# Kernel tuning notes

Measured on AMD Instinct MI355X. Metric: run time of the kernel, lower is better.

## Reference

```python
import jax, jax.numpy as jnp
import numpy as np

N_NODES = 50000
N_EDGES = 1600000
NFEAT = 512
NHID = 64
H1 = 8      # nheads[0]
H2 = 1      # nheads[1]
NCLASS = 16
ALPHA = 0.2  # leaky_relu negative slope


def setup_inputs() -> dict:
    key = jax.random.key(0)
    ks = jax.random.split(key, 6)
    x = jax.random.normal(ks[0], (N_NODES, NFEAT), jnp.float32)
    edge_index = jax.random.randint(ks[1], (2, N_EDGES), 0, N_NODES, jnp.int32)

    def glorot(k, shape):
        fan_in, fan_out = shape[-2], shape[-1]
        std = (2.0 / (fan_in + fan_out)) ** 0.5
        return jax.random.normal(k, shape, jnp.float32) * std

    W1 = glorot(ks[2], (H1, NFEAT, NHID))
    a1 = jax.random.normal(ks[3], (H1, 2 * NHID), jnp.float32) * 0.1
    W2 = glorot(ks[4], (H2, NHID * H1, NCLASS))
    a2 = jax.random.normal(ks[5], (H2, 2 * NCLASS), jnp.float32) * 0.1
    return {"x": x, "edge_index": edge_index, "W1": W1, "a1": a1, "W2": W2, "a2": a2}


def _spgat_head(x, W, a, src, dst, n_nodes, apply_elu):
    # Sparse GAT head (pyGAT SpGraphAttentionLayer, eval mode / no dropout).
    h = x @ W                              # [N, F']
    f = W.shape[1]
    # a . [h_src || h_dst] decomposed into per-node scores (same math, no [E,2F'] concat)
    s_src = h @ a[:f]                      # [N]
    s_dst = h @ a[f:]                      # [N]
    logits = s_src[src] + s_dst[dst]       # [E]
    e = jnp.exp(-jax.nn.leaky_relu(logits, ALPHA))  # edge_e = exp(-leakyrelu(...)) > 0
    rowsum = jax.ops.segment_sum(e, src, num_segments=n_nodes)            # [N]
    agg = jax.ops.segment_sum(e[:, None] * h[dst], src, num_segments=n_nodes)  # [N, F']
    h_prime = agg / rowsum[:, None]
    return jax.nn.elu(h_prime) if apply_elu else h_prime


def reference(x, edge_index, W1, a1, W2, a2):
    src, dst = edge_index[0], edge_index[1]
    n = x.shape[0]
    # Layer 1: H1 heads, concat=True (elu inside each head), concatenated on features
    h = jnp.concatenate(
        [_spgat_head(x, W1[i], a1[i], src, dst, n, True) for i in range(W1.shape[0])],
        axis=1,
    )  # [N, H1*NHID]
    # Layer 2: H2 heads, concat=False, stacked then averaged
    outs = jnp.stack(
        [_spgat_head(h, W2[i], a2[i], src, dst, n, False) for i in range(W2.shape[0])],
        axis=2,
    )  # [N, NCLASS, H2]
    out = jnp.mean(outs, axis=2)
    return jax.nn.log_softmax(jax.nn.elu(out), axis=1)
```

## Files before the change

### kernel.cpp

```cpp
#include <hip/hip_runtime.h>

#define NN 50000
#define NE 1600000
#define NFEAT 512
#define NHID 64
#define H1 8
#define NCLASS 16
#define ALPHA 0.2f

#define BUCKETS 391
#define CAP 6144
#define EPB 4096
#define PASSA_BLKS 391
#define PASSB_BLKS 391
#define PACK_BLKS 1024
#define PACK2_BLKS 32
#define GEMM_BLKS (4 * 391)

typedef __attribute__((ext_vector_type(8))) short short8;
typedef __attribute__((ext_vector_type(4))) float floatx4;
typedef __attribute__((ext_vector_type(2))) float floatx2;

__device__ __forceinline__ float elu_f(float x) { return x > 0.0f ? x : expf(x) - 1.0f; }
__device__ __forceinline__ float edge_w(float logit) {
    return expf(-fmaxf(logit, ALPHA * logit));
}
__device__ __forceinline__ ushort f2bf(float f) {
    uint u = __float_as_uint(f);
    return (ushort)((u + 0x7FFFu + ((u >> 16) & 1)) >> 16);
}
__device__ __forceinline__ uint packbf2(float lo, float hi) {
    return (uint)f2bf(lo) | ((uint)f2bf(hi) << 16);
}
__device__ __forceinline__ float bf2f(ushort v) { return __uint_as_float((uint)v << 16); }
__device__ __forceinline__ unsigned char f2fp8(float v) {
    return (unsigned char)(__builtin_amdgcn_cvt_pk_fp8_f32(v, v, 0, false) & 0xFF);
}
__device__ __forceinline__ uint pack4fp8(float a, float b, float c, float d) {
    uint u = __builtin_amdgcn_cvt_pk_fp8_f32(a, b, 0, false);
    return __builtin_amdgcn_cvt_pk_fp8_f32(c, d, u, true);
}

__device__ __forceinline__ int scan256x(int v, int tid, int* wsum, int* tot) {
    int s = v;
#pragma unroll
    for (int o = 1; o < 64; o <<= 1) {
        int u = __shfl_up(s, o);
        if ((tid & 63) >= o) s += u;
    }
    __syncthreads();
    if ((tid & 63) == 63) wsum[tid >> 6] = s;
    __syncthreads();
    int off = 0, t = 0;
#pragma unroll
    for (int i = 0; i < 4; i++) {
        int x = wsum[i];
        if (i < (tid >> 6)) off += x;
        t += x;
    }
    *tot = t;
    return s - v + off;
}

__global__ __launch_bounds__(256) void prep_k(const float* __restrict__ W1,
                                              unsigned char* __restrict__ Wt8,
                                              const float* __restrict__ W2,
                                              ushort* __restrict__ W2tb,
                                              const int* __restrict__ ei,
                                              int* __restrict__ bucket_cnt,
                                              uint* __restrict__ staging) {
    int b = blockIdx.x;
    if (b < PACK_BLKS) {
        int i = b * 256 + threadIdx.x;
        int c = i >> 9, k = i & 511;
        Wt8[i] = f2fp8(W1[((c >> 6) * 512 + k) * 64 + (c & 63)]);
        return;
    }
    if (b < PACK_BLKS + PACK2_BLKS) {
        int i = (b - PACK_BLKS) * 256 + threadIdx.x;
        int c = i >> 9, f = i & 511;
        W2tb[i] = f2bf(W2[f * 16 + c]);
        return;
    }
    __shared__ int histA[BUCKETS];
    __shared__ int exclA[BUCKETS];
    __shared__ int baseA[BUCKETS];
    __shared__ int wsumA[4];
    __shared__ uint ebuf[EPB];
    const int blk = b - PACK_BLKS - PACK2_BLKS;
    const int t = threadIdx.x;
    const int e0 = blk * EPB;
    const int cntb = min(EPB, NE - e0);
    for (int i = t; i < BUCKETS; i += 256) histA[i] = 0;
    __syncthreads();
    int br[16]; uint pay[16];
#pragma unroll
    for (int i = 0; i < 16; i++) {
        int e = e0 + i * 256 + t;
        br[i] = -1;
        if (e < NE) {
            int s = ei[e], d = ei[NE + e];
            int bu = s >> 7;
            pay[i] = ((uint)bu << 23) | ((uint)(s & 127) << 16) | (uint)d;
            br[i] = (bu << 12) | atomicAdd(&histA[bu], 1);
        }
    }
    __syncthreads();
    int tot0, tot1;
    int v0 = histA[t];
    int v1 = (t + 256 < BUCKETS) ? histA[t + 256] : 0;
    int p0 = scan256x(v0, t, wsumA, &tot0);
    int p1 = scan256x(v1, t, wsumA, &tot1);
    exclA[t] = p0;
    if (t + 256 < BUCKETS) exclA[t + 256] = p1 + tot0;
    __syncthreads();
    for (int i = t; i < BUCKETS; i += 256) {
        int c = histA[i];
        if (c > 0) baseA[i] = atomicAdd(&bucket_cnt[i], c);
    }
#pragma unroll
    for (int i = 0; i < 16; i++)
        if (br[i] >= 0) ebuf[exclA[br[i] >> 12] + (br[i] & 4095)] = pay[i];
    __syncthreads();
    for (int j = t; j < cntb; j += 256) {
        uint v = ebuf[j];
        int bu = v >> 23;
        int pos = baseA[bu] + (j - exclA[bu]);
        staging[(size_t)bu * CAP + pos] = v;
    }
}

__global__ __launch_bounds__(64) void scan_k(const int* __restrict__ bucket_cnt,
                                             int* __restrict__ bucket_start,
                                             int* __restrict__ rowptr) {
    const int lane = threadIdx.x;
    int c[7]; int s0 = 0;
#pragma unroll
    for (int i = 0; i < 7; i++) {
        int b = lane * 7 + i;
        c[i] = (b < BUCKETS) ? bucket_cnt[b] : 0;
        s0 += c[i];
    }
    int sc = s0;
#pragma unroll
    for (int o = 1; o < 64; o <<= 1) {
        int u = __shfl_up(sc, o);
        if (lane >= o) sc += u;
    }
    int run = sc - s0;
#pragma unroll
    for (int i = 0; i < 7; i++) {
        int b = lane * 7 + i;
        if (b < BUCKETS) bucket_start[b] = run;
        run += c[i];
    }
    if (lane == 63) { bucket_start[BUCKETS] = run; rowptr[NN] = run; }
}

__global__ __launch_bounds__(256) void passb_gemm1_k(const int* __restrict__ bucket_cnt,
                                                     const int* __restrict__ bucket_start,
                                                     const uint* __restrict__ staging,
                                                     ushort* __restrict__ csru,
                                                     int* __restrict__ rowptr,
                                                     const float* __restrict__ x,
                                                     const unsigned char* __restrict__ Wt8,
                                                     const float* __restrict__ a1,
                                                     unsigned char* __restrict__ h8,
                                                     float* __restrict__ s1s,
                                                     float* __restrict__ s1d) {
    __shared__ unsigned char As[128 * 32];
    __shared__ unsigned char Bs[128 * 32];
    const int tid = threadIdx.x;

    if (blockIdx.x < PASSB_BLKS) {
        __shared__ int hist2[128], excl2[128], cur2[128], wsum2[4];
        const int b = blockIdx.x;
        const int cnt = bucket_cnt[b];
        const int sbase = bucket_start[b];
        const uint* sg = staging + (size_t)b * CAP;
        if (tid < 128) { hist2[tid] = 0; cur2[tid] = 0; }
        __syncthreads();
        for (int e = tid; e < cnt; e += 256) atomicAdd(&hist2[(sg[e] >> 16) & 127], 1);
        __syncthreads();
        int v = (tid < 128) ? hist2[tid] : 0;
        int tot;
        int ex = scan256x(v, tid, wsum2, &tot);
        if (tid < 128) {
            excl2[tid] = ex;
            int n = b * 128 + tid;
            if (n < NN) rowptr[n] = sbase + ex;
        }
        __syncthreads();
        for (int e = tid; e < cnt; e += 256) {
            uint u = sg[e];
            int sl = (u >> 16) & 127;
            int pos = excl2[sl] + atomicAdd(&cur2[sl], 1);
            csru[sbase + pos] = (ushort)(u & 0xFFFF);
        }
        return;
    }

    const int gb = blockIdx.x - PASSB_BLKS;
    const int col0 = (gb & 3) * 128;
    const int row0 = (gb >> 2) * 128;
    const int wv = tid >> 6, lane = tid & 63;
    const int quad = lane >> 4, l16 = lane & 15;
    const int sm = tid >> 2, sk = (tid & 3) * 8;
    floatx4 acc[2][8];
#pragma unroll
    for (int rt = 0; rt < 2; rt++)
#pragma unroll
        for (int ct = 0; ct < 8; ct++) acc[rt][ct] = (floatx4){0.f, 0.f, 0.f, 0.f};

    for (int k0 = 0; k0 < 512; k0 += 32) {
#pragma unroll
        for (int p = 0; p < 2; p++) {
            int r = row0 + sm + p * 64;
            float4 f0 = {}, f1 = {};
            if (r < NN) {
                const float* xp = x + (size_t)r * 512 + k0 + sk;
                f0 = *(const float4*)xp;
                f1 = *(const float4*)(xp + 4);
            }
            uint2 av;
            av.x = pack4fp8(f0.x, f0.y, f0.z, f0.w);
            av.y = pack4fp8(f1.x, f1.y, f1.z, f1.w);
            *(uint2*)(As + (sm + p * 64) * 32 + sk) = av;
            int c = col0 + sm + p * 64;
            uint2 bv = *(const uint2*)(Wt8 + (size_t)c * 512 + k0 + sk);
            *(uint2*)(Bs + (sm + p * 64) * 32 + sk) = bv;
        }
        __syncthreads();
        long a0 = *(const long*)(As + (wv * 32 + l16) * 32 + quad * 8);
        long a1f = *(const long*)(As + (wv * 32 + 16 + l16) * 32 + quad * 8);
#pragma unroll
        for (int ct = 0; ct < 8; ct++) {
            long bf = *(const long*)(Bs + (ct * 16 + l16) * 32 + quad * 8);
            acc[0][ct] = __builtin_amdgcn_mfma_f32_16x16x32_fp8_fp8(a0, bf, acc[0][ct], 0, 0, 0);
            acc[1][ct] = __builtin_amdgcn_mfma_f32_16x16x32_fp8_fp8(a1f, bf, acc[1][ct], 0, 0, 0);
        }
        __syncthreads();
    }

#pragma unroll
    for (int rt = 0; rt < 2; rt++) {
        const int rbase = row0 + wv * 32 + rt * 16 + quad * 4;
        float ss[2][4] = {}, sd[2][4] = {};
#pragma unroll
        for (int ct = 0; ct < 8; ct++) {
            int colg = col0 + ct * 16 + l16;
            int head = colg >> 6;
            int hh = ct >> 2;
            float avs = a1[head * 128 + (colg & 63)];
            float avd = a1[head * 128 + 64 + (colg & 63)];
#pragma unroll
            for (int r = 0; r < 4; r++) {
                float v = acc[rt][ct][r];
                ss[hh][r] += v * avs;
                sd[hh][r] += v * avd;
                int row = rbase + r;
                if (row < NN) h8[(size_t)row * 512 + colg] = f2fp8(v);
            }
        }
#pragma unroll
        for (int hh = 0; hh < 2; hh++)
#pragma unroll
            for (int r = 0; r < 4; r++) {
                float a_ = ss[hh][r], b_ = sd[hh][r];
#pragma unroll
                for (int o = 1; o < 16; o <<= 1) {
                    a_ += __shfl_xor(a_, o);
                    b_ += __shfl_xor(b_, o);
                }
                int row = rbase + r;
                if (l16 == 0 && row < NN) {
                    int head = (col0 >> 6) + hh;
                    s1s[row * 8 + head] = a_;
                    s1d[row * 8 + head] = b_;
                }
            }
    }
}

__global__ __launch_bounds__(256) void agg1f_k(const int* __restrict__ rowptr,
                                               const ushort* __restrict__ csru,
                                               const float* __restrict__ s1s,
                                               const float* __restrict__ s1d,
                                               const uint2* __restrict__ hb8,
                                               const ushort* __restrict__ W2tb,
                                               const float* __restrict__ a2,
                                               ushort* __restrict__ h2b,
                                               float* __restrict__ s2s,
                                               float* __restrict__ s2d) {
    __shared__ ushort Ash[16 * 512];
    const int tid = threadIdx.x;
    const int wv = tid >> 6, lane = tid & 63;
    const int n0 = blockIdx.x * 4;
    const int n = n0 + wv;
    const int head8 = lane >> 3;
    const int esub = lane & 7;
    const int beg = rowptr[n];
    const int deg = rowptr[n + 1] - beg;
    const float ssrc = s1s[n * 8 + head8];
    floatx2 acc[4] = {};
    float rsum = 0.f;

    int k = 0;
    for (; k + 8 <= deg; k += 8) {
        int dA = csru[beg + k + esub];
        float wA = edge_w(ssrc + s1d[dA * 8 + head8]);
        rsum += wA;
        int dj[8];
#pragma unroll
        for (int j = 0; j < 8; j++) dj[j] = __shfl(dA, j);
        uint2 v[8];
#pragma unroll
        for (int j = 0; j < 8; j++) v[j] = hb8[(uint)dj[j] * 64 + lane];
#pragma unroll
        for (int j = 0; j < 8; j++) {
            float wj = __shfl(wA, (head8 << 3) + j);
            floatx2 w2 = (floatx2){wj, wj};
            acc[0] += w2 * __builtin_amdgcn_cvt_pk_f32_fp8(v[j].x, false);
            acc[1] += w2 * __builtin_amdgcn_cvt_pk_f32_fp8(v[j].x, true);
            acc[2] += w2 * __builtin_amdgcn_cvt_pk_f32_fp8(v[j].y, false);
            acc[3] += w2 * __builtin_amdgcn_cvt_pk_f32_fp8(v[j].y, true);
        }
    }
    if (k < deg) {
        int jc = min(k + esub, deg - 1);
        int dwj = csru[beg + jc];
        float w = edge_w(ssrc + s1d[dwj * 8 + head8]);
        if (k + esub >= deg) w = 0.f;
        rsum += w;
        int rem = deg - k;
        for (int j = 0; j < rem; j++) {
            int djs = __shfl(dwj, j);
            uint2 vv = hb8[(uint)djs * 64 + lane];
            float wj = __shfl(w, (head8 << 3) + j);
            floatx2 w2 = (floatx2){wj, wj};
            acc[0] += w2 * __builtin_amdgcn_cvt_pk_f32_fp8(vv.x, false);
            acc[1] += w2 * __builtin_amdgcn_cvt_pk_f32_fp8(vv.x, true);
            acc[2] += w2 * __builtin_amdgcn_cvt_pk_f32_fp8(vv.y, false);
            acc[3] += w2 * __builtin_amdgcn_cvt_pk_f32_fp8(vv.y, true);
        }
    }

    rsum += __shfl_xor(rsum, 1);
    rsum += __shfl_xor(rsum, 2);
    rsum += __shfl_xor(rsum, 4);
    float inv = 1.0f / rsum;
    uint4 o;
    o.x = packbf2(elu_f(acc[0][0] * inv), elu_f(acc[0][1] * inv));
    o.y = packbf2(elu_f(acc[1][0] * inv), elu_f(acc[1][1] * inv));
    o.z = packbf2(elu_f(acc[2][0] * inv), elu_f(acc[2][1] * inv));
    o.w = packbf2(elu_f(acc[3][0] * inv), elu_f(acc[3][1] * inv));
    *(uint4*)(Ash + wv * 512 + lane * 8) = o;
    __syncthreads();

    if (wv == 0) {
        const int l16 = lane & 15, q = lane >> 4;
        floatx4 c2 = (floatx4){0.f, 0.f, 0.f, 0.f};
#pragma unroll
        for (int s = 0; s < 16; s++) {
            short8 af = *(const short8*)(Ash + l16 * 512 + s * 32 + q * 8);
            short8 bf = *(const short8*)(W2tb + l16 * 512 + s * 32 + q * 8);
            c2 = __builtin_amdgcn_mfma_f32_16x16x32_bf16(af, bf, c2, 0, 0, 0);
        }
        if (q == 0) {
#pragma unroll
            for (int r = 0; r < 4; r++) h2b[(size_t)(n0 + r) * 16 + l16] = f2bf(c2[r]);
        }
#pragma unroll
        for (int r = 0; r < 4; r++) {
            float ssv = c2[r] * a2[l16];
            float sdv = c2[r] * a2[16 + l16];
#pragma unroll
            for (int oo = 1; oo < 16; oo <<= 1) {
                ssv += __shfl_xor(ssv, oo);
                sdv += __shfl_xor(sdv, oo);
            }
            if (lane == 0) { s2s[n0 + r] = ssv; s2d[n0 + r] = sdv; }
        }
    }
}

__global__ __launch_bounds__(256) void agg2_k(const int* __restrict__ rowptr,
                                              const ushort* __restrict__ csru,
                                              const float* __restrict__ s2s,
                                              const float* __restrict__ s2d,
                                              const ushort* __restrict__ h2b,
                                              float* __restrict__ out) {
    const int n = (blockIdx.x * 256 + threadIdx.x) >> 6;
    const int lane = threadIdx.x & 63;
    if (n >= NN) return;
    const int beg = rowptr[n], end = rowptr[n + 1];
    const float sn = s2s[n];
    const int sub = lane >> 4, f = lane & 15;
    float acc = 0.f, rsum = 0.f;
    int e = beg + sub;
    for (; e + 12 < end; e += 16) {
        int d0 = csru[e], d1 = csru[e + 4], d2 = csru[e + 8], d3 = csru[e + 12];
        float t0 = s2d[d0], t1 = s2d[d1], t2 = s2d[d2], t3 = s2d[d3];
        float g0 = bf2f(h2b[(uint)d0 * 16 + f]), g1 = bf2f(h2b[(uint)d1 * 16 + f]);
        float g2 = bf2f(h2b[(uint)d2 * 16 + f]), g3 = bf2f(h2b[(uint)d3 * 16 + f]);
        float w0 = edge_w(sn + t0), w1 = edge_w(sn + t1);
        float w2 = edge_w(sn + t2), w3 = edge_w(sn + t3);
        acc += w0 * g0 + w1 * g1 + w2 * g2 + w3 * g3;
        rsum += w0 + w1 + w2 + w3;
    }
    for (; e < end; e += 4) {
        int d0 = csru[e];
        float w0 = edge_w(sn + s2d[d0]);
        acc += w0 * bf2f(h2b[(uint)d0 * 16 + f]);
        rsum += w0;
    }
    acc += __shfl_down(acc, 32);
    acc += __shfl_down(acc, 16);
    rsum += __shfl_down(rsum, 32);
    rsum += __shfl_down(rsum, 16);
    if (lane < 16) {
        float v = elu_f(acc / rsum);
        float m = v;
#pragma unroll
        for (int o = 8; o > 0; o >>= 1) m = fmaxf(m, __shfl_xor(m, o));
        float ex = expf(v - m), s = ex;
#pragma unroll
        for (int o = 8; o > 0; o >>= 1) s += __shfl_xor(s, o);
        out[(size_t)n * 16 + f] = v - (logf(s) + m);
    }
}

extern "C" void kernel_launch(void* const* d_in, const int* in_sizes, int n_in,
                              void* d_out, int out_size, void* d_ws, size_t ws_size,
                              hipStream_t stream) {
    const float* x  = (const float*)d_in[0];
    const int*   ei = (const int*)d_in[1];
    const float* W1 = (const float*)d_in[2];
    const float* a1 = (const float*)d_in[3];
    const float* W2 = (const float*)d_in[4];
    const float* a2 = (const float*)d_in[5];
    float* out = (float*)d_out;

    unsigned char* h8  = (unsigned char*)d_ws;
    unsigned char* Wt8 = h8 + (size_t)NN * 512;
    ushort* W2tb  = (ushort*)(Wt8 + 512 * 512);
    float* s1s    = (float*)(W2tb + 8192);
    float* s1d    = s1s + (size_t)NN * H1;
    int* rowptr   = (int*)(s1d + (size_t)NN * H1);
    int* bucket_cnt   = rowptr + 50056;
    int* bucket_start = bucket_cnt + 512;
    ushort* csru  = (ushort*)(bucket_start + 512);
    ushort* h2b   = csru + NE;
    float* s2s    = (float*)(h2b + (size_t)NN * 16);
    float* s2d    = s2s + NN;
    uint* staging = (uint*)(s2d + NN);

    hipMemsetAsync(bucket_cnt, 0, 512 * sizeof(int), stream);

    prep_k<<<PACK_BLKS + PACK2_BLKS + PASSA_BLKS, 256, 0, stream>>>(W1, Wt8, W2, W2tb,
                                                                    ei, bucket_cnt, staging);
    scan_k<<<1, 64, 0, stream>>>(bucket_cnt, bucket_start, rowptr);
    passb_gemm1_k<<<PASSB_BLKS + GEMM_BLKS, 256, 0, stream>>>(bucket_cnt, bucket_start,
                                                              staging, csru, rowptr,
                                                              x, Wt8, a1, h8, s1s, s1d);
    agg1f_k<<<NN / 4, 256, 0, stream>>>(rowptr, csru, s1s, s1d,
                                        (const uint2*)h8, W2tb, a2, h2b, s2s, s2d);
    agg2_k<<<(NN + 3) / 4, 256, 0, stream>>>(rowptr, csru, s2s, s2d, h2b, out);
}
```

Before: 430.7 us.

## Pre-convert x to swizzled fp8 and restructure GEMM1 with direct-to-LDS loads

Adds a prep stage that converts x to fp8 once, in an XOR-swizzled layout, into the h8 buffer. The first GEMM is restructured so each 512-thread block computes all 512 output columns for 128 rows, with K-steps of 64, using global_load_lds to stream A and B tiles straight into shared memory. It then writes h8 in place over the x8 buffer. The aim is to stop re-reading and re-converting fp32 x for each column block and to cut LDS bank conflicts, at the cost of an extra fp8 write and read pass plus 128 accumulator registers per thread, which lowers occupancy.

```diff
diff --git a/kernel.cpp b/kernel.cpp
--- a/kernel.cpp
+++ b/kernel.cpp
@@ -15,11 +15,14 @@
 #define PASSB_BLKS 391
 #define PACK_BLKS 1024
 #define PACK2_BLKS 32
-#define GEMM_BLKS (4 * 391)
+#define X8_BLKS 6250
+#define GEMMB 391
+#define NROW_PAD 50048
 
 typedef __attribute__((ext_vector_type(8))) short short8;
 typedef __attribute__((ext_vector_type(4))) float floatx4;
 typedef __attribute__((ext_vector_type(2))) float floatx2;
+typedef __attribute__((ext_vector_type(2))) long longx2;
 
 __device__ __forceinline__ float elu_f(float x) { return x > 0.0f ? x : expf(x) - 1.0f; }
 __device__ __forceinline__ float edge_w(float logit) {
@@ -40,6 +43,11 @@
     uint u = __builtin_amdgcn_cvt_pk_fp8_f32(a, b, 0, false);
     return __builtin_amdgcn_cvt_pk_fp8_f32(c, d, u, true);
 }
+
+#define GLD16(g, l)                                                              \
+    __builtin_amdgcn_global_load_lds(                                            \
+        (const __attribute__((address_space(1))) unsigned int*)(g),              \
+        (__attribute__((address_space(3))) unsigned int*)(l), 16, 0, 0)
 
 __device__ __forceinline__ int scan256x(int v, int tid, int* wsum, int* tot) {
     int s = v;
@@ -62,17 +70,43 @@
     return s - v + off;
 }
 
+__device__ __forceinline__ int scan512x(int v, int tid, int* wsum, int* tot) {
+    int s = v;
+#pragma unroll
+    for (int o = 1; o < 64; o <<= 1) {
+        int u = __shfl_up(s, o);
+        if ((tid & 63) >= o) s += u;
+    }
+    __syncthreads();
+    if ((tid & 63) == 63) wsum[tid >> 6] = s;
+    __syncthreads();
+    int off = 0, t = 0;
+#pragma unroll
+    for (int i = 0; i < 8; i++) {
+        int x = wsum[i];
+        if (i < (tid >> 6)) off += x;
+        t += x;
+    }
+    *tot = t;
+    return s - v + off;
+}
+
 __global__ __launch_bounds__(256) void prep_k(const float* __restrict__ W1,
                                               unsigned char* __restrict__ Wt8,
                                               const float* __restrict__ W2,
                                               ushort* __restrict__ W2tb,
+                                              const float* __restrict__ x,
+                                              unsigned char* x8,
                                               const int* __restrict__ ei,
                                               int* __restrict__ bucket_cnt,
                                               uint* __restrict__ staging) {
     int b = blockIdx.x;
     if (b < PACK_BLKS) {
         int i = b * 256 + threadIdx.x;
-        int c = i >> 9, k = i & 511;
+        int c = i >> 9, o = i & 511;
+        int c6 = o >> 6, qhi = (o >> 4) & 3, kb = (o >> 3) & 1, bb = o & 7;
+        int quad = qhi ^ ((c >> 1) & 3);
+        int k = c6 * 64 + kb * 32 + quad * 8 + bb;
         Wt8[i] = f2fp8(W1[((c >> 6) * 512 + k) * 64 + (c & 63)]);
         return;
     }
@@ -82,12 +116,32 @@
         W2tb[i] = f2bf(W2[f * 16 + c]);
         return;
     }
+    if (b < PACK_BLKS + PACK2_BLKS + X8_BLKS) {
+        int i = (b - PACK_BLKS - PACK2_BLKS) * 256 + threadIdx.x;
+        int row = i >> 5;
+        int o0 = (i & 31) * 16;
+        int c6 = o0 >> 6;
+        int qhi = (o0 >> 4) & 3;
+        int quad = qhi ^ ((row >> 1) & 3);
+        const float* xp = x + (size_t)row * 512 + c6 * 64 + quad * 8;
+        float4 v0 = *(const float4*)xp;
+        float4 v1 = *(const float4*)(xp + 4);
+        float4 v2 = *(const float4*)(xp + 32);
+        float4 v3 = *(const float4*)(xp + 36);
+        uint4 ov;
+        ov.x = pack4fp8(v0.x, v0.y, v0.z, v0.w);
+        ov.y = pack4fp8(v1.x, v1.y, v1.z, v1.w);
+        ov.z = pack4fp8(v2.x, v2.y, v2.z, v2.w);
+        ov.w = pack4fp8(v3.x, v3.y, v3.z, v3.w);
+        *(uint4*)(x8 + (size_t)row * 512 + o0) = ov;
+        return;
+    }
     __shared__ int histA[BUCKETS];
     __shared__ int exclA[BUCKETS];
     __shared__ int baseA[BUCKETS];
     __shared__ int wsumA[4];
     __shared__ uint ebuf[EPB];
-    const int blk = b - PACK_BLKS - PACK2_BLKS;
+    const int blk = b - PACK_BLKS - PACK2_BLKS - X8_BLKS;
     const int t = threadIdx.x;
     const int e0 = blk * EPB;
     const int cntb = min(EPB, NE - e0);
@@ -157,41 +211,42 @@
     if (lane == 63) { bucket_start[BUCKETS] = run; rowptr[NN] = run; }
 }
 
-__global__ __launch_bounds__(256) void passb_gemm1_k(const int* __restrict__ bucket_cnt,
+__global__ __launch_bounds__(512) void passb_gemm1_k(const int* __restrict__ bucket_cnt,
                                                      const int* __restrict__ bucket_start,
                                                      const uint* __restrict__ staging,
                                                      ushort* __restrict__ csru,
                                                      int* __restrict__ rowptr,
-                                                     const float* __restrict__ x,
                                                      const unsigned char* __restrict__ Wt8,
                                                      const float* __restrict__ a1,
-                                                     unsigned char* __restrict__ h8,
+                                                     unsigned char* h8x8,
                                                      float* __restrict__ s1s,
                                                      float* __restrict__ s1d) {
-    __shared__ unsigned char As[128 * 32];
-    __shared__ unsigned char Bs[128 * 32];
+    __shared__ unsigned char shmem[40960];
     const int tid = threadIdx.x;
 
     if (blockIdx.x < PASSB_BLKS) {
-        __shared__ int hist2[128], excl2[128], cur2[128], wsum2[4];
+        int* hist2 = (int*)shmem;
+        int* excl2 = hist2 + 128;
+        int* cur2 = excl2 + 128;
+        int* wsum2 = cur2 + 128;
         const int b = blockIdx.x;
         const int cnt = bucket_cnt[b];
         const int sbase = bucket_start[b];
         const uint* sg = staging + (size_t)b * CAP;
         if (tid < 128) { hist2[tid] = 0; cur2[tid] = 0; }
         __syncthreads();
-        for (int e = tid; e < cnt; e += 256) atomicAdd(&hist2[(sg[e] >> 16) & 127], 1);
+        for (int e = tid; e < cnt; e += 512) atomicAdd(&hist2[(sg[e] >> 16) & 127], 1);
         __syncthreads();
         int v = (tid < 128) ? hist2[tid] : 0;
         int tot;
-        int ex = scan256x(v, tid, wsum2, &tot);
+        int ex = scan512x(v, tid, wsum2, &tot);
         if (tid < 128) {
             excl2[tid] = ex;
             int n = b * 128 + tid;
             if (n < NN) rowptr[n] = sbase + ex;
         }
         __syncthreads();
-        for (int e = tid; e < cnt; e += 256) {
+        for (int e = tid; e < cnt; e += 512) {
             uint u = sg[e];
             int sl = (u >> 16) & 127;
             int pos = excl2[sl] + atomicAdd(&cur2[sl], 1);
@@ -200,85 +255,76 @@
         return;
     }
 
+    unsigned char* As = shmem;
+    unsigned char* Bs = shmem + 8192;
     const int gb = blockIdx.x - PASSB_BLKS;
-    const int col0 = (gb & 3) * 128;
-    const int row0 = (gb >> 2) * 128;
+    const int row0 = gb * 128;
     const int wv = tid >> 6, lane = tid & 63;
-    const int quad = lane >> 4, l16 = lane & 15;
-    const int sm = tid >> 2, sk = (tid & 3) * 8;
-    floatx4 acc[2][8];
-#pragma unroll
-    for (int rt = 0; rt < 2; rt++)
-#pragma unroll
-        for (int ct = 0; ct < 8; ct++) acc[rt][ct] = (floatx4){0.f, 0.f, 0.f, 0.f};
-
-    for (int k0 = 0; k0 < 512; k0 += 32) {
-#pragma unroll
-        for (int p = 0; p < 2; p++) {
-            int r = row0 + sm + p * 64;
-            float4 f0 = {}, f1 = {};
-            if (r < NN) {
-                const float* xp = x + (size_t)r * 512 + k0 + sk;
-                f0 = *(const float4*)xp;
-                f1 = *(const float4*)(xp + 4);
+    const int l16 = lane & 15, quad = lane >> 4;
+    const int qoff = ((quad ^ ((l16 >> 1) & 3)) << 4);
+    const int mA = wv * 16 + (lane >> 2);
+    const int offA = (lane & 3) * 16;
+    const unsigned char* gA = h8x8 + (size_t)(row0 + mA) * 512 + offA;
+    const unsigned char* gB0 = Wt8 + (size_t)(0 * 128 + mA) * 512 + offA;
+    const unsigned char* gB1 = Wt8 + (size_t)(1 * 128 + mA) * 512 + offA;
+    const unsigned char* gB2 = Wt8 + (size_t)(2 * 128 + mA) * 512 + offA;
+    const unsigned char* gB3 = Wt8 + (size_t)(3 * 128 + mA) * 512 + offA;
+
+    floatx4 acc[32];
+#pragma unroll
+    for (int ct = 0; ct < 32; ct++) acc[ct] = (floatx4){0.f, 0.f, 0.f, 0.f};
+
+    for (int k0 = 0; k0 < 512; k0 += 64) {
+        GLD16(gA + k0, As + wv * 1024);
+        GLD16(gB0 + k0, Bs + wv * 1024);
+        GLD16(gB1 + k0, Bs + 8192 + wv * 1024);
+        GLD16(gB2 + k0, Bs + 16384 + wv * 1024);
+        GLD16(gB3 + k0, Bs + 24576 + wv * 1024);
+        __syncthreads();
+        longx2 av = *(const longx2*)(As + (wv * 16 + l16) * 64 + qoff);
+        const unsigned char* bp = Bs + l16 * 64 + qoff;
+#pragma unroll
+        for (int ct = 0; ct < 32; ct++) {
+            longx2 bv = *(const longx2*)(bp + ct * 1024);
+            acc[ct] = __builtin_amdgcn_mfma_f32_16x16x32_fp8_fp8(av.x, bv.x, acc[ct], 0, 0, 0);
+            acc[ct] = __builtin_amdgcn_mfma_f32_16x16x32_fp8_fp8(av.y, bv.y, acc[ct], 0, 0, 0);
+        }
+        __syncthreads();
+    }
+
+    const int rbase = row0 + wv * 16 + quad * 4;
+#pragma unroll
+    for (int hh = 0; hh < 8; hh++) {
+        float ss[4] = {0.f, 0.f, 0.f, 0.f}, sd[4] = {0.f, 0.f, 0.f, 0.f};
+#pragma unroll
+        for (int c4 = 0; c4 < 4; c4++) {
+            int ct = hh * 4 + c4;
+            int colg = ct * 16 + l16;
+            float avs = a1[hh * 128 + c4 * 16 + l16];
+            float avd = a1[hh * 128 + 64 + c4 * 16 + l16];
+#pragma unroll
+            for (int r = 0; r < 4; r++) {
+                float v = acc[ct][r];
+                ss[r] += v * avs;
+                sd[r] += v * avd;
+                int row = rbase + r;
+                if (row < NN) h8x8[(size_t)row * 512 + colg] = f2fp8(v);
             }
-            uint2 av;
-            av.x = pack4fp8(f0.x, f0.y, f0.z, f0.w);
-            av.y = pack4fp8(f1.x, f1.y, f1.z, f1.w);
-            *(uint2*)(As + (sm + p * 64) * 32 + sk) = av;
-            int c = col0 + sm + p * 64;
-            uint2 bv = *(const uint2*)(Wt8 + (size_t)c * 512 + k0 + sk);
-            *(uint2*)(Bs + (sm + p * 64) * 32 + sk) = bv;
-        }
-        __syncthreads();
-        long a0 = *(const long*)(As + (wv * 32 + l16) * 32 + quad * 8);
-        long a1f = *(const long*)(As + (wv * 32 + 16 + l16) * 32 + quad * 8);
-#pragma unroll
-        for (int ct = 0; ct < 8; ct++) {
-            long bf = *(const long*)(Bs + (ct * 16 + l16) * 32 + quad * 8);
-            acc[0][ct] = __builtin_amdgcn_mfma_f32_16x16x32_fp8_fp8(a0, bf, acc[0][ct], 0, 0, 0);
-            acc[1][ct] = __builtin_amdgcn_mfma_f32_16x16x32_fp8_fp8(a1f, bf, acc[1][ct], 0, 0, 0);
-        }
-        __syncthreads();
-    }
-
-#pragma unroll
-    for (int rt = 0; rt < 2; rt++) {
-        const int rbase = row0 + wv * 32 + rt * 16 + quad * 4;
-        float ss[2][4] = {}, sd[2][4] = {};
-#pragma unroll
-        for (int ct = 0; ct < 8; ct++) {
-            int colg = col0 + ct * 16 + l16;
-            int head = colg >> 6;
-            int hh = ct >> 2;
-            float avs = a1[head * 128 + (colg & 63)];
-            float avd = a1[head * 128 + 64 + (colg & 63)];
-#pragma unroll
-            for (int r = 0; r < 4; r++) {
-                float v = acc[rt][ct][r];
-                ss[hh][r] += v * avs;
-                sd[hh][r] += v * avd;
-                int row = rbase + r;
-                if (row < NN) h8[(size_t)row * 512 + colg] = f2fp8(v);
+        }
+#pragma unroll
+        for (int r = 0; r < 4; r++) {
+            float a_ = ss[r], b_ = sd[r];
+#pragma unroll
+            for (int o = 1; o < 16; o <<= 1) {
+                a_ += __shfl_xor(a_, o);
+                b_ += __shfl_xor(b_, o);
             }
-        }
-#pragma unroll
-        for (int hh = 0; hh < 2; hh++)
-#pragma unroll
-            for (int r = 0; r < 4; r++) {
-                float a_ = ss[hh][r], b_ = sd[hh][r];
-#pragma unroll
-                for (int o = 1; o < 16; o <<= 1) {
-                    a_ += __shfl_xor(a_, o);
-                    b_ += __shfl_xor(b_, o);
-                }
-                int row = rbase + r;
-                if (l16 == 0 && row < NN) {
-                    int head = (col0 >> 6) + hh;
-                    s1s[row * 8 + head] = a_;
-                    s1d[row * 8 + head] = b_;
-                }
+            int row = rbase + r;
+            if (l16 == 0 && row < NN) {
+                s1s[row * 8 + hh] = a_;
+                s1d[row * 8 + hh] = b_;
             }
+        }
     }
 }
 
@@ -442,7 +488,7 @@
     float* out = (float*)d_out;
 
     unsigned char* h8  = (unsigned char*)d_ws;
-    unsigned char* Wt8 = h8 + (size_t)NN * 512;
+    unsigned char* Wt8 = h8 + (size_t)NROW_PAD * 512;
     ushort* W2tb  = (ushort*)(Wt8 + 512 * 512);
     float* s1s    = (float*)(W2tb + 8192);
     float* s1d    = s1s + (size_t)NN * H1;
@@ -457,12 +503,12 @@
 
     hipMemsetAsync(bucket_cnt, 0, 512 * sizeof(int), stream);
 
-    prep_k<<<PACK_BLKS + PACK2_BLKS + PASSA_BLKS, 256, 0, stream>>>(W1, Wt8, W2, W2tb,
-                                                                    ei, bucket_cnt, staging);
+    prep_k<<<PACK_BLKS + PACK2_BLKS + X8_BLKS + PASSA_BLKS, 256, 0, stream>>>(
+        W1, Wt8, W2, W2tb, x, h8, ei, bucket_cnt, staging);
     scan_k<<<1, 64, 0, stream>>>(bucket_cnt, bucket_start, rowptr);
-    passb_gemm1_k<<<PASSB_BLKS + GEMM_BLKS, 256, 0, stream>>>(bucket_cnt, bucket_start,
-                                                              staging, csru, rowptr,
-                                                              x, Wt8, a1, h8, s1s, s1d);
+    passb_gemm1_k<<<PASSB_BLKS + GEMMB, 512, 0, stream>>>(bucket_cnt, bucket_start,
+                                                          staging, csru, rowptr,
+                                                          Wt8, a1, h8, s1s, s1d);
     agg1f_k<<<NN / 4, 256, 0, stream>>>(rowptr, csru, s1s, s1d,
                                         (const uint2*)h8, W2tb, a2, h2b, s2s, s2d);
     agg2_k<<<(NN + 3) / 4, 256, 0, stream>>>(rowptr, csru, s2s, s2d, h2b, out);
```

New measurement: 401.4 us. 6.8% less time.
